# Kernel tuning notes

Hardware: AMD Instinct MI355X
Metric: run time of the kernel (lower is better)

The kernel has to match this reference:

```python
import jax, jax.numpy as jnp
import numpy as np

HIDDEN = 512
HEADS = 8
HEAD_DIM = HIDDEN // HEADS
BATCH = 4096
SEQ = 16


def setup_inputs() -> dict:
    key = jax.random.key(0)
    k1, k2, k3 = jax.random.split(key, 3)
    scale = 1.0 / np.sqrt(HIDDEN)
    return {
        "hidden_states": jax.random.normal(k1, (BATCH, SEQ, HIDDEN), dtype=jnp.float32),
        # torch Linear(hidden, 3*hidden, bias=False): weight shape [3*hidden, hidden]
        "w_qkv": jax.random.uniform(k2, (3 * HIDDEN, HIDDEN), dtype=jnp.float32, minval=-scale, maxval=scale),
        "w_o": jax.random.uniform(k3, (HIDDEN, HIDDEN), dtype=jnp.float32, minval=-scale, maxval=scale),
    }


def reference(hidden_states, w_qkv, w_o):
    b, s, _ = hidden_states.shape
    # fused QKV projection: y = x @ W^T
    qkv = jnp.einsum("bsh,oh->bso", hidden_states, w_qkv)
    qkv = qkv.reshape(b, s, 3, HEADS, HEAD_DIM)
    qkv = jnp.transpose(qkv, (2, 0, 3, 1, 4))  # [3, b, heads, s, head_dim]
    q, k, v = qkv[0], qkv[1], qkv[2]
    # scaled dot-product attention (non-causal, dropout=0 in eval)
    scores = jnp.einsum("bhqd,bhkd->bhqk", q, k) / jnp.sqrt(jnp.float32(HEAD_DIM))
    probs = jax.nn.softmax(scores, axis=-1)
    attn = jnp.einsum("bhqk,bhkd->bhqd", probs, v)
    attn = jnp.transpose(attn, (0, 2, 1, 3)).reshape(b, s, HIDDEN)
    return jnp.einsum("bsh,oh->bso", attn, w_o)
```

## Files before the change

kernel.cpp:

```cpp
#include <hip/hip_runtime.h>


#define HID 512

typedef __attribute__((ext_vector_type(4))) float  float4v;
typedef __attribute__((ext_vector_type(8))) short  short8;
typedef __attribute__((ext_vector_type(4))) short  short4v;
typedef __attribute__((ext_vector_type(8))) __bf16 bf16x8;

static __device__ __forceinline__ short bf16rne(float f) {
    union { float f; unsigned u; } v; v.f = f;
    unsigned u = v.u + 0x7FFFu + ((v.u >> 16) & 1u);
    return (short)(u >> 16);
}

static __device__ __forceinline__ short8 pack8(float4v a, float4v b) {
    short8 o;
    o[0] = bf16rne(a[0]); o[1] = bf16rne(a[1]); o[2] = bf16rne(a[2]); o[3] = bf16rne(a[3]);
    o[4] = bf16rne(b[0]); o[5] = bf16rne(b[1]); o[6] = bf16rne(b[2]); o[7] = bf16rne(b[3]);
    return o;
}

static __device__ __forceinline__ void cvt8_store(short* dst, const float* src) {
    float4v a = *(const float4v*)src;
    float4v b = *(const float4v*)(src + 4);
    *(short8*)dst = pack8(a, b);
}

static __device__ __forceinline__ float4v mfma16(short8 a, short8 b, float4v c) {
    union { short8 s; bf16x8 v; } ua, ub;
    ua.s = a; ub.s = b;
    return __builtin_amdgcn_mfma_f32_16x16x32_bf16(ua.v, ub.v, c, 0, 0, 0);
}

static __device__ __forceinline__ void gld16(const short* g, short* l) {
    __builtin_amdgcn_global_load_lds(
        (const __attribute__((address_space(1))) void*)g,
        (__attribute__((address_space(3))) void*)l,
        16, 0, 0);
}

__global__ void cvt_kernel(const float* __restrict__ src, short* __restrict__ dst, int n4) {
    int i = blockIdx.x * 256 + threadIdx.x;
    if (i >= n4) return;
    float4v v = *(const float4v*)(src + (size_t)i * 4);
    short4v o;
    o[0] = bf16rne(v[0]); o[1] = bf16rne(v[1]); o[2] = bf16rne(v[2]); o[3] = bf16rne(v[3]);
    *(short4v*)(dst + (size_t)i * 4) = o;
}

__global__ __launch_bounds__(512, 4)
void qkv_head_kernel(const float* __restrict__ x, const short* __restrict__ xb, const int use_xb,
                     const float* __restrict__ wqf, const short* __restrict__ wqb, const int use_wb,
                     short* __restrict__ attnb, float* __restrict__ attnf, const int use_ab) {
    __shared__ __align__(16) union {
        struct { short a[128 * 64]; short b[192 * 64]; } st;
        struct { short q[128 * 72]; short k[128 * 72]; short vt[64 * 152]; short p[8 * 16 * 40]; } at;
    } L;

    const int tid  = threadIdx.x;
    const int wave = tid >> 6;
    const int lane = tid & 63;
    const int ln   = lane & 15;
    const int q8   = (lane >> 4) * 8;
    const int qrow = (lane >> 4) * 4;
    const int wr   = wave >> 2;
    const int wc   = wave & 3;

    const int g   = blockIdx.x;
    const int xcd = g & 7;
    const int j   = g >> 3;
    const int h   = j & 7;
    const int mt  = (j >> 3) * 8 + xcd;
    const int m0  = mt * 128;

    float4v acc[4][3];
    #pragma unroll
    for (int fr = 0; fr < 4; ++fr)
        #pragma unroll
        for (int fc = 0; fc < 3; ++fc)
            acc[fr][fc] = (float4v){0.f, 0.f, 0.f, 0.f};

    for (int kb = 0; kb < 8; ++kb) {
        __syncthreads();
        if (use_xb) {
            #pragma unroll
            for (int i = 0; i < 2; ++i) {
                const int cg  = i * 512 + tid;
                const int row = cg >> 3, c8 = (cg & 7) * 8;
                gld16(&xb[(size_t)(m0 + row) * HID + kb * 64 + c8],
                      &L.st.a[(size_t)(i * 512 + (wave << 6)) * 8]);
            }
        } else {
            #pragma unroll
            for (int i = 0; i < 2; ++i) {
                const int cg  = i * 512 + tid;
                const int row = cg >> 3, c8 = (cg & 7) * 8;
                cvt8_store(&L.st.a[(size_t)cg * 8], &x[(size_t)(m0 + row) * HID + kb * 64 + c8]);
            }
        }
        if (use_wb) {
            #pragma unroll
            for (int i = 0; i < 3; ++i) {
                const int cg   = i * 512 + tid;
                const int n    = cg >> 3, c8 = (cg & 7) * 8;
                const int grow = (n >> 6) * HID + h * 64 + (n & 63);
                gld16(&wqb[(size_t)grow * HID + kb * 64 + c8],
                      &L.st.b[(size_t)(i * 512 + (wave << 6)) * 8]);
            }
        } else {
            #pragma unroll
            for (int i = 0; i < 3; ++i) {
                const int cg   = i * 512 + tid;
                const int n    = cg >> 3, c8 = (cg & 7) * 8;
                const int grow = (n >> 6) * HID + h * 64 + (n & 63);
                cvt8_store(&L.st.b[(size_t)cg * 8], &wqf[(size_t)grow * HID + kb * 64 + c8]);
            }
        }
        __syncthreads();
        #pragma unroll
        for (int ks = 0; ks < 2; ++ks) {
            const int ko = ks * 32 + q8;
            short8 a[4], b[3];
            #pragma unroll
            for (int fr = 0; fr < 4; ++fr)
                a[fr] = *(const short8*)&L.st.a[(wr * 64 + fr * 16 + ln) * 64 + ko];
            #pragma unroll
            for (int fc = 0; fc < 3; ++fc)
                b[fc] = *(const short8*)&L.st.b[(wc * 48 + fc * 16 + ln) * 64 + ko];
            #pragma unroll
            for (int fr = 0; fr < 4; ++fr)
                #pragma unroll
                for (int fc = 0; fc < 3; ++fc)
                    acc[fr][fc] = mfma16(a[fr], b[fc], acc[fr][fc]);
        }
    }
    __syncthreads();

    #pragma unroll
    for (int fr = 0; fr < 4; ++fr) {
        #pragma unroll
        for (int fc = 0; fc < 3; ++fc) {
            const int nb = wc * 48 + fc * 16;
            const int n  = nb + ln;
            const int mb = wr * 64 + fr * 16 + qrow;
            const float4v v = acc[fr][fc];
            if (nb < 64) {
                #pragma unroll
                for (int r = 0; r < 4; ++r)
                    L.at.q[(mb + r) * 72 + n] = bf16rne(v[r] * 0.125f);
            } else if (nb < 128) {
                #pragma unroll
                for (int r = 0; r < 4; ++r)
                    L.at.k[(mb + r) * 72 + (n - 64)] = bf16rne(v[r]);
            } else {
                #pragma unroll
                for (int r = 0; r < 4; ++r)
                    L.at.vt[(n - 128) * 152 + mb + r] = bf16rne(v[r]);
            }
        }
    }
    for (int i = tid; i < 64 * 24; i += 512)
        L.at.vt[(i / 24) * 152 + 128 + (i % 24)] = 0;
    for (int i = tid; i < 8 * 16 * 16; i += 512)
        L.at.p[(i >> 8) * 640 + ((i >> 4) & 15) * 40 + 16 + (i & 15)] = 0;
    __syncthreads();

    {
        const int rb = wave * 16;
        const short* qp = &L.at.q[(rb + ln) * 72 + q8];
        const short* kp = &L.at.k[(rb + ln) * 72 + q8];
        short8 aq0 = *(const short8*)qp;
        short8 aq1 = *(const short8*)(qp + 32);
        short8 bk0 = *(const short8*)kp;
        short8 bk1 = *(const short8*)(kp + 32);
        float4v s = (float4v){0.f, 0.f, 0.f, 0.f};
        s = mfma16(aq0, bk0, s);
        s = mfma16(aq1, bk1, s);

        float4v mx = s;
        #pragma unroll
        for (int off = 1; off < 16; off <<= 1)
            #pragma unroll
            for (int r = 0; r < 4; ++r)
                mx[r] = fmaxf(mx[r], __shfl_xor(mx[r], off));
        float4v p;
        #pragma unroll
        for (int r = 0; r < 4; ++r) p[r] = __expf(s[r] - mx[r]);
        float4v sm = p;
        #pragma unroll
        for (int off = 1; off < 16; off <<= 1)
            #pragma unroll
            for (int r = 0; r < 4; ++r)
                sm[r] += __shfl_xor(sm[r], off);
        #pragma unroll
        for (int r = 0; r < 4; ++r)
            L.at.p[wave * 640 + (qrow + r) * 40 + ln] = bf16rne(p[r] * __builtin_amdgcn_rcpf(sm[r]));

        short8 ap = *(const short8*)&L.at.p[wave * 640 + ln * 40 + q8];
        #pragma unroll
        for (int dc = 0; dc < 4; ++dc) {
            short8 bv = *(const short8*)&L.at.vt[(dc * 16 + ln) * 152 + rb + q8];
            float4v o = (float4v){0.f, 0.f, 0.f, 0.f};
            o = mfma16(ap, bv, o);
            #pragma unroll
            for (int r = 0; r < 4; ++r) {
                const size_t oi = (size_t)(m0 + rb + qrow + r) * HID + h * 64 + dc * 16 + ln;
                if (use_ab) attnb[oi] = bf16rne(o[r]);
                else        attnf[oi] = o[r];
            }
        }
    }
}

__global__ __launch_bounds__(256, 4)
void oproj_kernel(const short* __restrict__ attnb,
                  const float* __restrict__ wof, const short* __restrict__ wob,
                  const int use_wb, float* __restrict__ out) {
    __shared__ __align__(16) short A[128 * 64];
    __shared__ __align__(16) short B[128 * 64];

    const int tid  = threadIdx.x;
    const int wave = tid >> 6;
    const int lane = tid & 63;
    const int ln   = lane & 15;
    const int q8   = (lane >> 4) * 8;
    const int qrow = (lane >> 4) * 4;
    const int wr   = wave >> 1;
    const int wc   = wave & 1;

    const int g   = blockIdx.x;
    const int xcd = g & 7;
    const int j   = g >> 3;
    const int nt  = j & 3;
    const int mt  = (j >> 2) * 8 + xcd;
    const int m0  = mt * 128;
    const int n0  = nt * 128;

    float4v acc[4][4];
    #pragma unroll
    for (int fr = 0; fr < 4; ++fr)
        #pragma unroll
        for (int fc = 0; fc < 4; ++fc)
            acc[fr][fc] = (float4v){0.f, 0.f, 0.f, 0.f};

    for (int kb = 0; kb < 8; ++kb) {
        __syncthreads();
        #pragma unroll
        for (int i = 0; i < 4; ++i) {
            const int cg  = i * 256 + tid;
            const int row = cg >> 3, c8 = (cg & 7) * 8;
            gld16(&attnb[(size_t)(m0 + row) * HID + kb * 64 + c8],
                  &A[(size_t)(i * 256 + (wave << 6)) * 8]);
            if (use_wb)
                gld16(&wob[(size_t)(n0 + row) * HID + kb * 64 + c8],
                      &B[(size_t)(i * 256 + (wave << 6)) * 8]);
            else
                cvt8_store(&B[(size_t)cg * 8], &wof[(size_t)(n0 + row) * HID + kb * 64 + c8]);
        }
        __syncthreads();
        #pragma unroll
        for (int ks = 0; ks < 2; ++ks) {
            const int ko = ks * 32 + q8;
            short8 a[4], b[4];
            #pragma unroll
            for (int fr = 0; fr < 4; ++fr)
                a[fr] = *(const short8*)&A[(wr * 64 + fr * 16 + ln) * 64 + ko];
            #pragma unroll
            for (int fc = 0; fc < 4; ++fc)
                b[fc] = *(const short8*)&B[(wc * 64 + fc * 16 + ln) * 64 + ko];
            #pragma unroll
            for (int fr = 0; fr < 4; ++fr)
                #pragma unroll
                for (int fc = 0; fc < 4; ++fc)
                    acc[fr][fc] = mfma16(a[fr], b[fc], acc[fr][fc]);
        }
    }
    #pragma unroll
    for (int fr = 0; fr < 4; ++fr)
        #pragma unroll
        for (int fc = 0; fc < 4; ++fc)
            #pragma unroll
            for (int r = 0; r < 4; ++r)
                out[(size_t)(m0 + wr * 64 + fr * 16 + qrow + r) * HID +
                    n0 + wc * 64 + fc * 16 + ln] = acc[fr][fc][r];
}

__global__ __launch_bounds__(512, 2)
void oproj_inplace_kernel(float* __restrict__ io, const float* __restrict__ wof,
                          const short* __restrict__ wob, const int use_wb) {
    __shared__ __align__(16) short sA[64 * 40];
    __shared__ __align__(16) short sW2[512 * 40];

    const int tid  = threadIdx.x;
    const int wave = tid >> 6;
    const int lane = tid & 63;
    const int ln   = lane & 15;
    const int q8   = (lane >> 4) * 8;
    const int qrow = (lane >> 4) * 4;
    const int m0   = blockIdx.x * 64;

    float4v acc[4][4];
    #pragma unroll
    for (int fr = 0; fr < 4; ++fr)
        #pragma unroll
        for (int fc = 0; fc < 4; ++fc)
            acc[fr][fc] = (float4v){0.f, 0.f, 0.f, 0.f};

    for (int kb = 0; kb < 16; ++kb) {
        __syncthreads();
        if (tid < 256) {
            int row = tid >> 2, c8 = (tid & 3) * 8;
            cvt8_store(&sA[row * 40 + c8], &io[(size_t)(m0 + row) * HID + kb * 32 + c8]);
        }
        #pragma unroll
        for (int it = 0; it < 4; ++it) {
            int gg = tid + it * 512;
            int n = gg >> 2, c8 = (gg & 3) * 8;
            if (use_wb)
                *(short8*)&sW2[n * 40 + c8] = *(const short8*)&wob[(size_t)n * HID + kb * 32 + c8];
            else
                cvt8_store(&sW2[n * 40 + c8], &wof[(size_t)n * HID + kb * 32 + c8]);
        }
        __syncthreads();
        short8 a[4], b[4];
        #pragma unroll
        for (int fr = 0; fr < 4; ++fr)
            a[fr] = *(const short8*)&sA[(fr * 16 + ln) * 40 + q8];
        #pragma unroll
        for (int fc = 0; fc < 4; ++fc)
            b[fc] = *(const short8*)&sW2[(wave * 64 + fc * 16 + ln) * 40 + q8];
        #pragma unroll
        for (int fr = 0; fr < 4; ++fr)
            #pragma unroll
            for (int fc = 0; fc < 4; ++fc)
                acc[fr][fc] = mfma16(a[fr], b[fc], acc[fr][fc]);
    }
    #pragma unroll
    for (int fr = 0; fr < 4; ++fr)
        #pragma unroll
        for (int fc = 0; fc < 4; ++fc)
            #pragma unroll
            for (int r = 0; r < 4; ++r)
                io[(size_t)(m0 + fr * 16 + qrow + r) * HID + wave * 64 + fc * 16 + ln] =
                    acc[fr][fc][r];
}

extern "C" void kernel_launch(void* const* d_in, const int* in_sizes, int n_in,
                              void* d_out, int out_size, void* d_ws, size_t ws_size,
                              hipStream_t stream) {
    const float* x    = (const float*)d_in[0];
    const float* wqkv = (const float*)d_in[1];
    const float* wo   = (const float*)d_in[2];
    float* out = (float*)d_out;

    const size_t n_x  = (size_t)65536 * HID;
    const size_t n_wq = (size_t)1536 * HID;
    const size_t n_wo = (size_t)HID * HID;
    const size_t szA = (n_x * 2 + n_wq + n_wo) * 2;
    const size_t szB = (n_x + n_wq + n_wo) * 2;
    const size_t szC = (n_wq + n_wo) * 2;

    short* xb = nullptr; short* attnb = nullptr; short* wqb = nullptr; short* wob = nullptr;
    int use_xb = 0, use_ab = 0, use_wb = 0;
    short* ws = (short*)d_ws;

    if (d_ws && ws_size >= szA) {
        use_xb = use_ab = use_wb = 1;
        xb = ws; attnb = xb + n_x; wqb = attnb + n_x; wob = wqb + n_wq;
    } else if (d_ws && ws_size >= szB) {
        use_ab = use_wb = 1;
        attnb = ws; wqb = attnb + n_x; wob = wqb + n_wq;
    } else if (d_ws && ws_size >= szC) {
        use_wb = 1;
        wqb = ws; wob = wqb + n_wq;
    }

    if (use_xb)
        cvt_kernel<<<(int)(n_x / 1024), 256, 0, stream>>>(x, xb, (int)(n_x / 4));
    if (use_wb) {
        cvt_kernel<<<(int)(n_wq / 1024), 256, 0, stream>>>(wqkv, wqb, (int)(n_wq / 4));
        cvt_kernel<<<(int)(n_wo / 1024), 256, 0, stream>>>(wo, wob, (int)(n_wo / 4));
    }

    qkv_head_kernel<<<4096, 512, 0, stream>>>(x, xb, use_xb, wqkv, wqb, use_wb,
                                              attnb, out , use_ab);

    if (use_ab)
        oproj_kernel<<<2048, 256, 0, stream>>>(attnb, wo, wob, use_wb, out);
    else
        oproj_inplace_kernel<<<1024, 512, 0, stream>>>(out, wo, wob, use_wb);
}
```

Measured before the change: 427.6 us.

## Double-buffer LDS staging in QKV and O-proj GEMMs; widen O-proj to 512 threads

Both GEMM main loops now use two LDS buffers, so the global-to-LDS loads for the next K block are issued before the MFMAs on the current block and each iteration needs one barrier instead of two. The aim is to hide global load latency behind compute. The O-projection kernel also moves from 256 to 512 threads, with each wave computing a 64x32 tile instead of 64x64. The costs are double the LDS staging footprint (QKV staging grows to 80KB, O-proj to 64KB), which may lower occupancy, and less register-level reuse per wave in O-proj.

```diff
diff --git a/kernel.cpp b/kernel.cpp
--- a/kernel.cpp
+++ b/kernel.cpp
@@ -54,7 +54,7 @@
                      const float* __restrict__ wqf, const short* __restrict__ wqb, const int use_wb,
                      short* __restrict__ attnb, float* __restrict__ attnf, const int use_ab) {
     __shared__ __align__(16) union {
-        struct { short a[128 * 64]; short b[192 * 64]; } st;
+        struct { short a[2][128 * 64]; short b[2][192 * 64]; } st;
         struct { short q[128 * 72]; short k[128 * 72]; short vt[64 * 152]; short p[8 * 16 * 40]; } at;
     } L;
 
@@ -81,24 +81,25 @@
         for (int fc = 0; fc < 3; ++fc)
             acc[fr][fc] = (float4v){0.f, 0.f, 0.f, 0.f};
 
-    for (int kb = 0; kb < 8; ++kb) {
-        __syncthreads();
+    auto stageA = [&](int buf, int kb) {
         if (use_xb) {
             #pragma unroll
             for (int i = 0; i < 2; ++i) {
                 const int cg  = i * 512 + tid;
                 const int row = cg >> 3, c8 = (cg & 7) * 8;
                 gld16(&xb[(size_t)(m0 + row) * HID + kb * 64 + c8],
-                      &L.st.a[(size_t)(i * 512 + (wave << 6)) * 8]);
+                      &L.st.a[buf][(i * 512 + (wave << 6)) * 8]);
             }
         } else {
             #pragma unroll
             for (int i = 0; i < 2; ++i) {
                 const int cg  = i * 512 + tid;
                 const int row = cg >> 3, c8 = (cg & 7) * 8;
-                cvt8_store(&L.st.a[(size_t)cg * 8], &x[(size_t)(m0 + row) * HID + kb * 64 + c8]);
-            }
-        }
+                cvt8_store(&L.st.a[buf][cg * 8], &x[(size_t)(m0 + row) * HID + kb * 64 + c8]);
+            }
+        }
+    };
+    auto stageB = [&](int buf, int kb) {
         if (use_wb) {
             #pragma unroll
             for (int i = 0; i < 3; ++i) {
@@ -106,7 +107,7 @@
                 const int n    = cg >> 3, c8 = (cg & 7) * 8;
                 const int grow = (n >> 6) * HID + h * 64 + (n & 63);
                 gld16(&wqb[(size_t)grow * HID + kb * 64 + c8],
-                      &L.st.b[(size_t)(i * 512 + (wave << 6)) * 8]);
+                      &L.st.b[buf][(i * 512 + (wave << 6)) * 8]);
             }
         } else {
             #pragma unroll
@@ -114,28 +115,40 @@
                 const int cg   = i * 512 + tid;
                 const int n    = cg >> 3, c8 = (cg & 7) * 8;
                 const int grow = (n >> 6) * HID + h * 64 + (n & 63);
-                cvt8_store(&L.st.b[(size_t)cg * 8], &wqf[(size_t)grow * HID + kb * 64 + c8]);
-            }
-        }
-        __syncthreads();
+                cvt8_store(&L.st.b[buf][cg * 8], &wqf[(size_t)grow * HID + kb * 64 + c8]);
+            }
+        }
+    };
+
+    stageA(0, 0);
+    stageB(0, 0);
+    __syncthreads();
+
+    int cur = 0;
+    for (int kb = 0; kb < 8; ++kb) {
+        if (kb < 7) {
+            stageA(cur ^ 1, kb + 1);
+            stageB(cur ^ 1, kb + 1);
+        }
         #pragma unroll
         for (int ks = 0; ks < 2; ++ks) {
             const int ko = ks * 32 + q8;
             short8 a[4], b[3];
             #pragma unroll
             for (int fr = 0; fr < 4; ++fr)
-                a[fr] = *(const short8*)&L.st.a[(wr * 64 + fr * 16 + ln) * 64 + ko];
+                a[fr] = *(const short8*)&L.st.a[cur][(wr * 64 + fr * 16 + ln) * 64 + ko];
             #pragma unroll
             for (int fc = 0; fc < 3; ++fc)
-                b[fc] = *(const short8*)&L.st.b[(wc * 48 + fc * 16 + ln) * 64 + ko];
+                b[fc] = *(const short8*)&L.st.b[cur][(wc * 48 + fc * 16 + ln) * 64 + ko];
             #pragma unroll
             for (int fr = 0; fr < 4; ++fr)
                 #pragma unroll
                 for (int fc = 0; fc < 3; ++fc)
                     acc[fr][fc] = mfma16(a[fr], b[fc], acc[fr][fc]);
         }
-    }
-    __syncthreads();
+        __syncthreads();
+        cur ^= 1;
+    }
 
     #pragma unroll
     for (int fr = 0; fr < 4; ++fr) {
@@ -213,12 +226,12 @@
     }
 }
 
-__global__ __launch_bounds__(256, 4)
+__global__ __launch_bounds__(512, 4)
 void oproj_kernel(const short* __restrict__ attnb,
                   const float* __restrict__ wof, const short* __restrict__ wob,
                   const int use_wb, float* __restrict__ out) {
-    __shared__ __align__(16) short A[128 * 64];
-    __shared__ __align__(16) short B[128 * 64];
+    __shared__ __align__(16) short A[2][128 * 64];
+    __shared__ __align__(16) short B[2][128 * 64];
 
     const int tid  = threadIdx.x;
     const int wave = tid >> 6;
@@ -226,8 +239,8 @@
     const int ln   = lane & 15;
     const int q8   = (lane >> 4) * 8;
     const int qrow = (lane >> 4) * 4;
-    const int wr   = wave >> 1;
-    const int wc   = wave & 1;
+    const int wr   = wave >> 2;
+    const int wc   = wave & 3;
 
     const int g   = blockIdx.x;
     const int xcd = g & 7;
@@ -237,53 +250,62 @@
     const int m0  = mt * 128;
     const int n0  = nt * 128;
 
-    float4v acc[4][4];
+    float4v acc[4][2];
     #pragma unroll
     for (int fr = 0; fr < 4; ++fr)
         #pragma unroll
-        for (int fc = 0; fc < 4; ++fc)
+        for (int fc = 0; fc < 2; ++fc)
             acc[fr][fc] = (float4v){0.f, 0.f, 0.f, 0.f};
 
-    for (int kb = 0; kb < 8; ++kb) {
-        __syncthreads();
-        #pragma unroll
-        for (int i = 0; i < 4; ++i) {
-            const int cg  = i * 256 + tid;
+    auto stage = [&](int buf, int kb) {
+        #pragma unroll
+        for (int i = 0; i < 2; ++i) {
+            const int cg  = i * 512 + tid;
             const int row = cg >> 3, c8 = (cg & 7) * 8;
             gld16(&attnb[(size_t)(m0 + row) * HID + kb * 64 + c8],
-                  &A[(size_t)(i * 256 + (wave << 6)) * 8]);
+                  &A[buf][(i * 512 + (wave << 6)) * 8]);
             if (use_wb)
                 gld16(&wob[(size_t)(n0 + row) * HID + kb * 64 + c8],
-                      &B[(size_t)(i * 256 + (wave << 6)) * 8]);
+                      &B[buf][(i * 512 + (wave << 6)) * 8]);
             else
-                cvt8_store(&B[(size_t)cg * 8], &wof[(size_t)(n0 + row) * HID + kb * 64 + c8]);
-        }
-        __syncthreads();
+                cvt8_store(&B[buf][cg * 8], &wof[(size_t)(n0 + row) * HID + kb * 64 + c8]);
+        }
+    };
+
+    stage(0, 0);
+    __syncthreads();
+
+    int cur = 0;
+    for (int kb = 0; kb < 8; ++kb) {
+        if (kb < 7) stage(cur ^ 1, kb + 1);
         #pragma unroll
         for (int ks = 0; ks < 2; ++ks) {
             const int ko = ks * 32 + q8;
-            short8 a[4], b[4];
+            short8 a[4], b[2];
             #pragma unroll
             for (int fr = 0; fr < 4; ++fr)
-                a[fr] = *(const short8*)&A[(wr * 64 + fr * 16 + ln) * 64 + ko];
-            #pragma unroll
-            for (int fc = 0; fc < 4; ++fc)
-                b[fc] = *(const short8*)&B[(wc * 64 + fc * 16 + ln) * 64 + ko];
+                a[fr] = *(const short8*)&A[cur][(wr * 64 + fr * 16 + ln) * 64 + ko];
+            #pragma unroll
+            for (int fc = 0; fc < 2; ++fc)
+                b[fc] = *(const short8*)&B[cur][(wc * 32 + fc * 16 + ln) * 64 + ko];
             #pragma unroll
             for (int fr = 0; fr < 4; ++fr)
                 #pragma unroll
-                for (int fc = 0; fc < 4; ++fc)
+                for (int fc = 0; fc < 2; ++fc)
                     acc[fr][fc] = mfma16(a[fr], b[fc], acc[fr][fc]);
         }
-    }
+        __syncthreads();
+        cur ^= 1;
+    }
+
     #pragma unroll
     for (int fr = 0; fr < 4; ++fr)
         #pragma unroll
-        for (int fc = 0; fc < 4; ++fc)
+        for (int fc = 0; fc < 2; ++fc)
             #pragma unroll
             for (int r = 0; r < 4; ++r)
                 out[(size_t)(m0 + wr * 64 + fr * 16 + qrow + r) * HID +
-                    n0 + wc * 64 + fc * 16 + ln] = acc[fr][fc][r];
+                    n0 + wc * 32 + fc * 16 + ln] = acc[fr][fc][r];
 }
 
 __global__ __launch_bounds__(512, 2)
@@ -387,7 +409,7 @@
                                               attnb, out , use_ab);
 
     if (use_ab)
-        oproj_kernel<<<2048, 256, 0, stream>>>(attnb, wo, wob, use_wb, out);
+        oproj_kernel<<<2048, 512, 0, stream>>>(attnb, wo, wob, use_wb, out);
     else
         oproj_inplace_kernel<<<1024, 512, 0, stream>>>(out, wo, wob, use_wb);
 }
```

After: 430.0 us. Within noise of the previous version (+0.6%).
